# Optimization experiments

Hardware: AMD Instinct MI355X
Metric: run time of the kernel (lower is better)

## Reference

```python
import jax, jax.numpy as jnp
import numpy as np
import math

NUM_BUCKETS = 32
MAX_DISTANCE = 128
N_HEADS = 16
D_KV = 64
ATTN_SCALE = True


def _relative_position_bucket(relative_position, num_buckets=NUM_BUCKETS, max_distance=MAX_DISTANCE):
    # bidirectional (encoder) variant
    nb = num_buckets // 2
    buckets = (relative_position > 0).astype(jnp.int32) * nb
    rp = jnp.abs(relative_position)
    max_exact = nb // 2
    is_small = rp < max_exact
    rp_large = max_exact + (
        jnp.log(rp.astype(jnp.float32) / max_exact)
        / math.log(max_distance / max_exact)
        * (nb - max_exact)
    ).astype(jnp.int32)
    rp_large = jnp.minimum(rp_large, nb - 1)
    buckets = buckets + jnp.where(is_small, rp, rp_large)
    return buckets


def compute_bias(rel_bias_emb, q_len, k_len):
    ctx = jnp.arange(q_len)[:, None]
    mem = jnp.arange(k_len)[None, :]
    bucket = _relative_position_bucket(mem - ctx)  # [q,k] int32 in [0,32)
    values = rel_bias_emb[bucket]                  # [q,k,H]
    return jnp.transpose(values, (2, 0, 1))[None]  # [1,H,q,k]


def setup_inputs() -> dict:
    key = jax.random.key(0)
    k1, k2, k3, k4 = jax.random.split(key, 4)
    B, S, D = 2, 2048, 1024
    return {
        "hidden_states": jax.random.normal(k1, (B, S, D), jnp.float32),
        "attention_mask": jnp.ones((B, 1, S, S), jnp.float32),
        "W_qkv": jax.random.normal(k2, (D, 3 * D), jnp.float32) * 0.02,
        "W_o": jax.random.normal(k3, (D, D), jnp.float32) * 0.02,
        "rel_bias_emb": jax.random.normal(k4, (NUM_BUCKETS, N_HEADS), jnp.float32) * 0.02,
    }


def reference(hidden_states, attention_mask, W_qkv, W_o, rel_bias_emb):
    B, S, D = hidden_states.shape
    # fused QKV projection (no bias), then split as in split_tensor_along_last_dim
    qkv = jnp.einsum("bsd,de->bse", hidden_states, W_qkv)
    q, k, v = jnp.split(qkv, 3, axis=-1)
    # [b,s,H*d] -> [b,H,s,d]
    def to_heads(t):
        return jnp.transpose(t.reshape(B, S, N_HEADS, D_KV), (0, 2, 1, 3))
    q, k, v = to_heads(q), to_heads(k), to_heads(v)
    scores = jnp.einsum("bhqd,bhkd->bhqk", q, k)
    if ATTN_SCALE:
        scores = scores / math.sqrt(D_KV)
    position_bias = compute_bias(rel_bias_emb, S, S)  # [1,H,S,S]
    scores = scores * attention_mask + (-10000.0 * (1.0 - attention_mask) + position_bias)
    probs = jax.nn.softmax(scores, axis=-1)  # dropout = eval mode (identity)
    ctx = jnp.einsum("bhqk,bhkd->bhqd", probs, v)
    ctx = jnp.transpose(ctx, (0, 2, 1, 3)).reshape(B, S, N_HEADS * D_KV)
    attn_output = jnp.einsum("bse,ed->bsd", ctx, W_o)
    return attn_output
```

## Files before the change

### kernel.cpp

```cpp
#include <hip/hip_runtime.h>
#include <cstdint>

#define DEV static __device__ __forceinline__

typedef __bf16 bf16x8 __attribute__((ext_vector_type(8)));
typedef __bf16 bf16x4 __attribute__((ext_vector_type(4)));
typedef short  s16x4  __attribute__((ext_vector_type(4)));
typedef float  f32x4  __attribute__((ext_vector_type(4)));

DEV unsigned short f32_bf16(float f) {
  union { float f; unsigned u; } v; v.f = f;
  unsigned r = v.u + 0x7FFFu + ((v.u >> 16) & 1u);
  return (unsigned short)(r >> 16);
}

DEV void gload16(const void* g, void* lds) {
  __builtin_amdgcn_global_load_lds((__attribute__((address_space(1))) void*)g,
                                   (__attribute__((address_space(3))) void*)lds,
                                   16, 0, 0);
}

DEV float bcast_lane(float v, int srclane) {
  union { float f; int i; } u; u.f = v;
  u.i = __builtin_amdgcn_ds_bpermute(srclane << 2, u.i);
  return u.f;
}

DEV f32x4 mfma16_bf16(bf16x4 a, bf16x4 b, f32x4 c) {
  union { bf16x4 h; s16x4 s; } ua, ub; ua.h = a; ub.h = b;
#if __has_builtin(__builtin_amdgcn_mfma_f32_16x16x16bf16_1k)
  return __builtin_amdgcn_mfma_f32_16x16x16bf16_1k(ua.s, ub.s, c, 0, 0, 0);
#else
  f32x4 d;
  asm("v_mfma_f32_16x16x16_bf16 %0, %1, %2, %3" : "=v"(d) : "v"(ua.s), "v"(ub.s), "v"(c));
  return d;
#endif
}

__global__ void cast_bf16(const float* __restrict__ x, unsigned short* __restrict__ y) {
  int i = blockIdx.x * 256 + threadIdx.x;
  float4 v = ((const float4*)x)[i];
  uint2 o;
  o.x = (unsigned)f32_bf16(v.x) | ((unsigned)f32_bf16(v.y) << 16);
  o.y = (unsigned)f32_bf16(v.z) | ((unsigned)f32_bf16(v.w) << 16);
  ((uint2*)y)[i] = o;
}

__global__ void transpose_cast(const float* __restrict__ W, unsigned short* __restrict__ WT,
                               int K, int N) {
  __shared__ float t[64][65];
  int k0 = blockIdx.x * 64, n0 = blockIdx.y * 64;
  int tn = threadIdx.x & 63, tk = threadIdx.x >> 6;
#pragma unroll
  for (int i = 0; i < 64; i += 4)
    t[tk + i][tn] = W[(size_t)(k0 + tk + i) * N + n0 + tn];
  __syncthreads();
  int k2 = (threadIdx.x & 31) * 2, n = threadIdx.x >> 5;
#pragma unroll
  for (int i = 0; i < 64; i += 8) {
    int nn = n + i;
    unsigned o = (unsigned)f32_bf16(t[k2][nn]) | ((unsigned)f32_bf16(t[k2 + 1][nn]) << 16);
    *(unsigned*)&WT[(size_t)(n0 + nn) * K + k0 + k2] = o;
  }
}

__global__ void mask_check(const float* __restrict__ m, int* __restrict__ flag) {
  size_t i = ((size_t)blockIdx.x * 256 + threadIdx.x) * 4;
  float4 v = *(const float4*)(m + i);
  if (v.x != 1.0f || v.y != 1.0f || v.z != 1.0f || v.w != 1.0f) atomicOr(flag, 1);
}

template <int MODE, int TN>
__global__ void __launch_bounds__(256) gemm_bt(const unsigned short* __restrict__ A,
                                               const unsigned short* __restrict__ BT,
                                               float* __restrict__ Cout,
                                               unsigned short* __restrict__ Qb,
                                               unsigned short* __restrict__ Kb,
                                               unsigned short* __restrict__ VTb,
                                               int M, int N, int K) {
  constexpr int NT = TN / 32;
  __shared__ __align__(16) unsigned short As[128 * 32];
  __shared__ __align__(16) unsigned short Bs[TN * 32];
  const int tid = threadIdx.x, wave = tid >> 6, lane = tid & 63;
  const int l = lane & 15, quad = lane >> 4;
  const int wm = (wave & 1) * 64, wn = (wave >> 1) * (TN >> 1);
  const int bm = blockIdx.x, bn = blockIdx.y;

  const int srowA = wave * 32 + (lane >> 2);
  const int sswzA = ((lane & 3) ^ (srowA & 3)) * 8;
  const int srowB = (TN == 128) ? srowA : (wave * 16 + (lane >> 2));
  const int sswzB = ((lane & 3) ^ (srowB & 3)) * 8;
  const unsigned short* pA = A + (size_t)(bm * 128 + srowA) * K + sswzA;
  const unsigned short* pB = BT + (size_t)(bn * TN + srowB) * K + sswzB;
  unsigned short* ldsA0 = &As[(wave * 32) * 32];
  unsigned short* ldsA1 = &As[(wave * 32 + 16) * 32];
  unsigned short* ldsB0 = &Bs[((TN == 128 ? wave * 32 : wave * 16)) * 32];
  unsigned short* ldsB1 = &Bs[(wave * 32 + 16) * 32];

  f32x4 acc[4][NT];
#pragma unroll
  for (int i = 0; i < 4; i++)
#pragma unroll
    for (int j = 0; j < NT; j++) { f32x4 z = {0.f, 0.f, 0.f, 0.f}; acc[i][j] = z; }

  for (int kt = 0; kt < K; kt += 32) {
    __syncthreads();
    gload16(pA, ldsA0);
    gload16(pA + (size_t)16 * K, ldsA1);
    gload16(pB, ldsB0);
    if (TN == 128) gload16(pB + (size_t)16 * K, ldsB1);
    pA += 32; pB += 32;
    __syncthreads();
    bf16x8 af[4], bv[NT];
#pragma unroll
    for (int mt = 0; mt < 4; mt++) {
      int r = wm + mt * 16 + l;
      af[mt] = *(const bf16x8*)&As[r * 32 + ((quad ^ (r & 3)) * 8)];
    }
#pragma unroll
    for (int nt = 0; nt < NT; nt++) {
      int r = wn + nt * 16 + l;
      bv[nt] = *(const bf16x8*)&Bs[r * 32 + ((quad ^ (r & 3)) * 8)];
    }
#pragma unroll
    for (int mt = 0; mt < 4; mt++)
#pragma unroll
      for (int nt = 0; nt < NT; nt++)
        acc[mt][nt] = __builtin_amdgcn_mfma_f32_16x16x32_bf16(af[mt], bv[nt], acc[mt][nt], 0, 0, 0);
  }

#pragma unroll
  for (int nt = 0; nt < NT; nt++) {
    const int col = bn * TN + wn + nt * 16 + l;
#pragma unroll
    for (int mt = 0; mt < 4; mt++) {
      const int row0 = bm * 128 + wm + mt * 16 + quad * 4;
      if (MODE == 0) {
#pragma unroll
        for (int r = 0; r < 4; r++)
          Cout[(size_t)(row0 + r) * N + col] = acc[mt][nt][r];
      } else {
        const int bb = row0 >> 11, s = row0 & 2047;
        if (col < 2048) {
          unsigned short* dst = (col < 1024) ? Qb : Kb;
          const int c = col & 1023;
          const size_t off = ((size_t)(bb * 16 + (c >> 6)) * 2048 + s) * 64 + (c & 63);
#pragma unroll
          for (int r = 0; r < 4; r++)
            dst[off + (size_t)r * 64] = f32_bf16(acc[mt][nt][r]);
        } else {
          const int c = col - 2048;
          const size_t off = ((size_t)(bb * 16 + (c >> 6)) * 64 + (c & 63)) * 2048 + s;
          bf16x4 pk;
#pragma unroll
          for (int r = 0; r < 4; r++) pk[r] = (__bf16)acc[mt][nt][r];
          *(bf16x4*)&VTb[off] = pk;
        }
      }
    }
  }
}

__global__ void __launch_bounds__(256, 2) attn(const unsigned short* __restrict__ Qb,
                                               const unsigned short* __restrict__ Kb,
                                               const unsigned short* __restrict__ VTb,
                                               const float* __restrict__ mask,
                                               const float* __restrict__ emb,
                                               const int* __restrict__ mflag,
                                               unsigned short* __restrict__ ctx) {
  __shared__ __align__(16) unsigned short KV[2][16384];
  __shared__ float biasLUT[512];

  const float LOG2E = 1.4426950408889634f;
  const float c1 = 0.125f * LOG2E;
  const float C2 = 10000.0f * LOG2E;
  const int tid = threadIdx.x, wave = tid >> 6, lane = tid & 63;
  const int l = lane & 15, quad = lane >> 4;
  const int qt = blockIdx.x & 15, bh = blockIdx.x >> 4;
  const int b = bh >> 4, h = bh & 15;
  const int q0 = qt * 128;

  for (int i = tid; i < 512; i += 256) {
    int rel = i - 256;
    int rp = rel < 0 ? -rel : rel;
    int off = rp < 8 ? rp
                     : 8 + (rp >= 12) + (rp >= 16) + (rp >= 23) + (rp >= 32) +
                           (rp >= 46) + (rp >= 64) + (rp >= 91);
    int bucket = (rel > 0 ? 16 : 0) + off;
    biasLUT[i] = emb[bucket * 16 + h] * LOG2E;
  }
  const float satL = emb[15 * 16 + h] * LOG2E;
  const float satH = emb[31 * 16 + h] * LOG2E;
  const int masked = *mflag;

  const unsigned short* qb  = Qb  + ((size_t)(b * 16 + h) * 2048 + q0) * 64;
  const unsigned short* kb  = Kb  + (size_t)(b * 16 + h) * 2048 * 64;
  const unsigned short* vtb = VTb + (size_t)(b * 16 + h) * 64 * 2048;
  const float* mbase = mask + (size_t)b * 2048 * 2048;

  const int rw8 = lane >> 3, c8 = lane & 7;
  const int rw16 = lane >> 4, c16 = lane & 15;

#pragma unroll
  for (int j = 0; j < 4; j++) {
    int row = wave * 32 + j * 8 + rw8;
    gload16(qb + (size_t)row * 64 + ((c8 ^ (row & 7)) * 8), &KV[1][(wave * 32 + j * 8) * 64]);
  }
#pragma unroll
  for (int j = 0; j < 4; j++) {
    int row = wave * 32 + j * 8 + rw8;
    gload16(kb + (size_t)row * 64 + ((c8 ^ (row & 7)) * 8), &KV[0][(wave * 32 + j * 8) * 64]);
  }
#pragma unroll
  for (int j = 0; j < 4; j++) {
    int drow = wave * 16 + j * 4 + rw16;
    gload16(vtb + (size_t)drow * 2048 + ((c16 ^ (drow & 7)) * 8),
            &KV[0][8192 + (wave * 16 + j * 4) * 128]);
  }
  __syncthreads();

  bf16x8 qf[2][2];
#pragma unroll
  for (int mtq = 0; mtq < 2; mtq++)
#pragma unroll
    for (int ks = 0; ks < 2; ks++) {
      int row = wave * 32 + mtq * 16 + l;
      qf[mtq][ks] = *(const bf16x8*)&KV[1][row * 64 + (((ks * 4 + quad) ^ (row & 7)) * 8)];
    }
  __syncthreads();

#pragma unroll
  for (int j = 0; j < 4; j++) {
    int row = wave * 32 + j * 8 + rw8;
    gload16(kb + (size_t)(128 + row) * 64 + ((c8 ^ (row & 7)) * 8),
            &KV[1][(wave * 32 + j * 8) * 64]);
  }
#pragma unroll
  for (int j = 0; j < 4; j++) {
    int drow = wave * 16 + j * 4 + rw16;
    gload16(vtb + (size_t)drow * 2048 + 128 + ((c16 ^ (drow & 7)) * 8),
            &KV[1][8192 + (wave * 16 + j * 4) * 128]);
  }

  float lr[2] = {0.f, 0.f};
  f32x4 Oa[2][4];
#pragma unroll
  for (int mt = 0; mt < 2; mt++)
#pragma unroll
    for (int dt = 0; dt < 4; dt++) { f32x4 z = {0.f, 0.f, 0.f, 0.f}; Oa[mt][dt] = z; }

  for (int kt = 0; kt < 16; kt++) {
    const int k0 = kt * 128;
    const unsigned short* Ks  = KV[kt & 1];
    const unsigned short* VTs = KV[kt & 1] + 8192;

    const int d0 = k0 - q0;
    const bool sat = (d0 >= 256) || (d0 <= -256);
    const float bias_u = d0 > 0 ? satH : satL;
    const int ibase = 256 + d0 + quad * 4 - wave * 32 - l;
    bf16x4 pa[2][8];

#pragma unroll
    for (int ntk = 0; ntk < 8; ntk++) {
      int row = ntk * 16 + l;
      bf16x8 kf0 = *(const bf16x8*)&Ks[row * 64 + ((quad ^ (row & 7)) * 8)];
      bf16x8 kf1 = *(const bf16x8*)&Ks[row * 64 + (((4 + quad) ^ (row & 7)) * 8)];
#pragma unroll
      for (int mtq = 0; mtq < 2; mtq++) {
        f32x4 s = {0.f, 0.f, 0.f, 0.f};
        s = __builtin_amdgcn_mfma_f32_16x16x32_bf16(kf0, qf[mtq][0], s, 0, 0, 0);
        s = __builtin_amdgcn_mfma_f32_16x16x32_bf16(kf1, qf[mtq][1], s, 0, 0, 0);

        const int ib = ibase - mtq * 16 + ntk * 16;
        if (!masked) {
          if (sat) {
#pragma unroll
            for (int r = 0; r < 4; r++) s[r] = fmaf(s[r], c1, bias_u);
          } else {
#pragma unroll
            for (int r = 0; r < 4; r++) s[r] = fmaf(s[r], c1, biasLUT[ib + r]);
          }
        } else {
          const int qg = q0 + wave * 32 + mtq * 16 + l;
          const int kg = k0 + ntk * 16 + quad * 4;
          float4 mv4 = *(const float4*)&mbase[(size_t)qg * 2048 + kg];
#pragma unroll
          for (int r = 0; r < 4; r++) {
            float mv = r == 0 ? mv4.x : (r == 1 ? mv4.y : (r == 2 ? mv4.z : mv4.w));
            float bias = sat ? bias_u : biasLUT[ib + r];
            s[r] = fmaf(s[r], mv * c1, fmaf(mv, C2, bias - C2));
          }
        }
        bf16x4 pk;
        float ls = 0.f;
#pragma unroll
        for (int r = 0; r < 4; r++) {
          float p = __builtin_amdgcn_exp2f(s[r]);
          ls += p;
          pk[r] = (__bf16)p;
        }
        lr[mtq] += ls;
        pa[mtq][ntk] = pk;
      }
    }

#pragma unroll
    for (int ntk = 0; ntk < 8; ntk++) {
      bf16x4 vf[4];
#pragma unroll
      for (int dt = 0; dt < 4; dt++) {
        int row = dt * 16 + l;
        int ch = (ntk * 2 + (quad >> 1)) ^ (l & 7);
        vf[dt] = *(const bf16x4*)&VTs[row * 128 + ch * 8 + (quad & 1) * 4];
      }
#pragma unroll
      for (int mtq = 0; mtq < 2; mtq++)
#pragma unroll
        for (int dt = 0; dt < 4; dt++)
          Oa[mtq][dt] = mfma16_bf16(pa[mtq][ntk], vf[dt], Oa[mtq][dt]);
    }

    __syncthreads();
    if (kt + 2 < 16) {
      const int kn = (kt + 2) * 128;
      unsigned short* dst = (unsigned short*)KV[kt & 1];
#pragma unroll
      for (int j = 0; j < 4; j++) {
        int row = wave * 32 + j * 8 + rw8;
        gload16(kb + (size_t)(kn + row) * 64 + ((c8 ^ (row & 7)) * 8),
                &dst[(wave * 32 + j * 8) * 64]);
      }
#pragma unroll
      for (int j = 0; j < 4; j++) {
        int drow = wave * 16 + j * 4 + rw16;
        gload16(vtb + (size_t)drow * 2048 + kn + ((c16 ^ (drow & 7)) * 8),
                &dst[8192 + (wave * 16 + j * 4) * 128]);
      }
    }
  }

  float inv[2];
#pragma unroll
  for (int mtq = 0; mtq < 2; mtq++) {
    float v = lr[mtq];
    v += __shfl_xor(v, 16);
    v += __shfl_xor(v, 32);
    inv[mtq] = 1.0f / v;
  }
#pragma unroll
  for (int mt = 0; mt < 2; mt++)
#pragma unroll
    for (int r = 0; r < 4; r++) {
      float i_bc = bcast_lane(inv[mt], quad * 4 + r);
      const int qg = q0 + wave * 32 + mt * 16 + quad * 4 + r;
#pragma unroll
      for (int dt = 0; dt < 4; dt++)
        ctx[(size_t)(b * 2048 + qg) * 1024 + h * 64 + dt * 16 + l] =
            f32_bf16(Oa[mt][dt][r] * i_bc);
    }
}

extern "C" void kernel_launch(void* const* d_in, const int* in_sizes, int n_in,
                              void* d_out, int out_size, void* d_ws, size_t ws_size,
                              hipStream_t stream) {
  const float* hs   = (const float*)d_in[0];
  const float* mask = (const float*)d_in[1];
  const float* wqkv = (const float*)d_in[2];
  const float* wo   = (const float*)d_in[3];
  const float* emb  = (const float*)d_in[4];
  float* out = (float*)d_out;

  char* ws = (char*)d_ws;
  unsigned short* hB  = (unsigned short*)(ws);
  unsigned short* ctx = (unsigned short*)(ws);
  unsigned short* wqT = (unsigned short*)(ws + 8388608);
  unsigned short* woT = (unsigned short*)(ws + 14680064);
  unsigned short* Qb  = (unsigned short*)(ws + 16777216);
  unsigned short* Kb  = (unsigned short*)(ws + 25165824);
  unsigned short* VTb = (unsigned short*)(ws + 33554432);
  int* mflag          = (int*)(ws + 41943040);
  if (ws_size < 41943044) return;

  hipMemsetAsync(mflag, 0, 4, stream);
  cast_bf16<<<4096, 256, 0, stream>>>(hs, hB);
  transpose_cast<<<dim3(16, 48), 256, 0, stream>>>(wqkv, wqT, 1024, 3072);
  transpose_cast<<<dim3(16, 16), 256, 0, stream>>>(wo, woT, 1024, 1024);
  mask_check<<<8192, 256, 0, stream>>>(mask, mflag);
  gemm_bt<2, 128><<<dim3(32, 24), 256, 0, stream>>>(hB, wqT, nullptr, Qb, Kb, VTb, 4096, 3072, 1024);
  attn<<<512, 256, 0, stream>>>(Qb, Kb, VTb, mask, emb, mflag, ctx);
  gemm_bt<0, 64><<<dim3(32, 16), 256, 0, stream>>>(ctx, woT, out, nullptr, nullptr, nullptr, 4096, 1024, 1024);
}
```

Measured before the change: 225.6 us.

## Use 8 waves per attention block with 16 query rows each and reorder block mapping

The attention kernel now launches 512 threads (8 waves) per block. Each wave handles 16 query rows instead of 32, so the per-wave Q fragments, P tiles and output accumulators are halved. The block index mapping is changed so that consecutive blocks cover different batch-heads at the same query tile rather than different query tiles of one head. The goal is more waves in flight to hide latency and a smaller register footprint. The cost is that each K/V tile loaded into LDS is reused by fewer rows per wave, and block-wide barriers now synchronise more waves.

```diff
diff --git a/kernel.cpp b/kernel.cpp
--- a/kernel.cpp
+++ b/kernel.cpp
@@ -161,7 +161,7 @@
   }
 }
 
-__global__ void __launch_bounds__(256, 2) attn(const unsigned short* __restrict__ Qb,
+__global__ void __launch_bounds__(512, 4) attn(const unsigned short* __restrict__ Qb,
                                                const unsigned short* __restrict__ Kb,
                                                const unsigned short* __restrict__ VTb,
                                                const float* __restrict__ mask,
@@ -176,11 +176,12 @@
   const float C2 = 10000.0f * LOG2E;
   const int tid = threadIdx.x, wave = tid >> 6, lane = tid & 63;
   const int l = lane & 15, quad = lane >> 4;
-  const int qt = blockIdx.x & 15, bh = blockIdx.x >> 4;
+  const int bh = blockIdx.x & 31, qt = blockIdx.x >> 5;
   const int b = bh >> 4, h = bh & 15;
   const int q0 = qt * 128;
 
-  for (int i = tid; i < 512; i += 256) {
+  {
+    int i = tid;
     int rel = i - 256;
     int rp = rel < 0 ? -rel : rel;
     int off = rp < 8 ? rp
@@ -202,52 +203,48 @@
   const int rw16 = lane >> 4, c16 = lane & 15;
 
 #pragma unroll
-  for (int j = 0; j < 4; j++) {
-    int row = wave * 32 + j * 8 + rw8;
-    gload16(qb + (size_t)row * 64 + ((c8 ^ (row & 7)) * 8), &KV[1][(wave * 32 + j * 8) * 64]);
-  }
-#pragma unroll
-  for (int j = 0; j < 4; j++) {
-    int row = wave * 32 + j * 8 + rw8;
-    gload16(kb + (size_t)row * 64 + ((c8 ^ (row & 7)) * 8), &KV[0][(wave * 32 + j * 8) * 64]);
-  }
-#pragma unroll
-  for (int j = 0; j < 4; j++) {
-    int drow = wave * 16 + j * 4 + rw16;
+  for (int j = 0; j < 2; j++) {
+    int row = wave * 16 + j * 8 + rw8;
+    gload16(qb + (size_t)row * 64 + ((c8 ^ (row & 7)) * 8), &KV[1][(wave * 16 + j * 8) * 64]);
+  }
+#pragma unroll
+  for (int j = 0; j < 2; j++) {
+    int row = wave * 16 + j * 8 + rw8;
+    gload16(kb + (size_t)row * 64 + ((c8 ^ (row & 7)) * 8), &KV[0][(wave * 16 + j * 8) * 64]);
+  }
+#pragma unroll
+  for (int j = 0; j < 2; j++) {
+    int drow = wave * 8 + j * 4 + rw16;
     gload16(vtb + (size_t)drow * 2048 + ((c16 ^ (drow & 7)) * 8),
-            &KV[0][8192 + (wave * 16 + j * 4) * 128]);
+            &KV[0][8192 + (wave * 8 + j * 4) * 128]);
   }
   __syncthreads();
 
-  bf16x8 qf[2][2];
-#pragma unroll
-  for (int mtq = 0; mtq < 2; mtq++)
-#pragma unroll
-    for (int ks = 0; ks < 2; ks++) {
-      int row = wave * 32 + mtq * 16 + l;
-      qf[mtq][ks] = *(const bf16x8*)&KV[1][row * 64 + (((ks * 4 + quad) ^ (row & 7)) * 8)];
-    }
+  bf16x8 qf[2];
+#pragma unroll
+  for (int ks = 0; ks < 2; ks++) {
+    int row = wave * 16 + l;
+    qf[ks] = *(const bf16x8*)&KV[1][row * 64 + (((ks * 4 + quad) ^ (row & 7)) * 8)];
+  }
   __syncthreads();
 
 #pragma unroll
-  for (int j = 0; j < 4; j++) {
-    int row = wave * 32 + j * 8 + rw8;
+  for (int j = 0; j < 2; j++) {
+    int row = wave * 16 + j * 8 + rw8;
     gload16(kb + (size_t)(128 + row) * 64 + ((c8 ^ (row & 7)) * 8),
-            &KV[1][(wave * 32 + j * 8) * 64]);
-  }
-#pragma unroll
-  for (int j = 0; j < 4; j++) {
-    int drow = wave * 16 + j * 4 + rw16;
+            &KV[1][(wave * 16 + j * 8) * 64]);
+  }
+#pragma unroll
+  for (int j = 0; j < 2; j++) {
+    int drow = wave * 8 + j * 4 + rw16;
     gload16(vtb + (size_t)drow * 2048 + 128 + ((c16 ^ (drow & 7)) * 8),
-            &KV[1][8192 + (wave * 16 + j * 4) * 128]);
-  }
-
-  float lr[2] = {0.f, 0.f};
-  f32x4 Oa[2][4];
-#pragma unroll
-  for (int mt = 0; mt < 2; mt++)
-#pragma unroll
-    for (int dt = 0; dt < 4; dt++) { f32x4 z = {0.f, 0.f, 0.f, 0.f}; Oa[mt][dt] = z; }
+            &KV[1][8192 + (wave * 8 + j * 4) * 128]);
+  }
+
+  float lr = 0.f;
+  f32x4 Oa[4];
+#pragma unroll
+  for (int dt = 0; dt < 4; dt++) { f32x4 z = {0.f, 0.f, 0.f, 0.f}; Oa[dt] = z; }
 
   for (int kt = 0; kt < 16; kt++) {
     const int k0 = kt * 128;
@@ -257,51 +254,48 @@
     const int d0 = k0 - q0;
     const bool sat = (d0 >= 256) || (d0 <= -256);
     const float bias_u = d0 > 0 ? satH : satL;
-    const int ibase = 256 + d0 + quad * 4 - wave * 32 - l;
-    bf16x4 pa[2][8];
+    const int ibase = 256 + d0 + quad * 4 - wave * 16 - l;
+    bf16x4 pa[8];
 
 #pragma unroll
     for (int ntk = 0; ntk < 8; ntk++) {
       int row = ntk * 16 + l;
       bf16x8 kf0 = *(const bf16x8*)&Ks[row * 64 + ((quad ^ (row & 7)) * 8)];
       bf16x8 kf1 = *(const bf16x8*)&Ks[row * 64 + (((4 + quad) ^ (row & 7)) * 8)];
-#pragma unroll
-      for (int mtq = 0; mtq < 2; mtq++) {
-        f32x4 s = {0.f, 0.f, 0.f, 0.f};
-        s = __builtin_amdgcn_mfma_f32_16x16x32_bf16(kf0, qf[mtq][0], s, 0, 0, 0);
-        s = __builtin_amdgcn_mfma_f32_16x16x32_bf16(kf1, qf[mtq][1], s, 0, 0, 0);
-
-        const int ib = ibase - mtq * 16 + ntk * 16;
-        if (!masked) {
-          if (sat) {
-#pragma unroll
-            for (int r = 0; r < 4; r++) s[r] = fmaf(s[r], c1, bias_u);
-          } else {
-#pragma unroll
-            for (int r = 0; r < 4; r++) s[r] = fmaf(s[r], c1, biasLUT[ib + r]);
-          }
+      f32x4 s = {0.f, 0.f, 0.f, 0.f};
+      s = __builtin_amdgcn_mfma_f32_16x16x32_bf16(kf0, qf[0], s, 0, 0, 0);
+      s = __builtin_amdgcn_mfma_f32_16x16x32_bf16(kf1, qf[1], s, 0, 0, 0);
+
+      const int ib = ibase + ntk * 16;
+      if (!masked) {
+        if (sat) {
+#pragma unroll
+          for (int r = 0; r < 4; r++) s[r] = fmaf(s[r], c1, bias_u);
         } else {
-          const int qg = q0 + wave * 32 + mtq * 16 + l;
-          const int kg = k0 + ntk * 16 + quad * 4;
-          float4 mv4 = *(const float4*)&mbase[(size_t)qg * 2048 + kg];
-#pragma unroll
-          for (int r = 0; r < 4; r++) {
-            float mv = r == 0 ? mv4.x : (r == 1 ? mv4.y : (r == 2 ? mv4.z : mv4.w));
-            float bias = sat ? bias_u : biasLUT[ib + r];
-            s[r] = fmaf(s[r], mv * c1, fmaf(mv, C2, bias - C2));
-          }
+#pragma unroll
+          for (int r = 0; r < 4; r++) s[r] = fmaf(s[r], c1, biasLUT[ib + r]);
         }
-        bf16x4 pk;
-        float ls = 0.f;
+      } else {
+        const int qg = q0 + wave * 16 + l;
+        const int kg = k0 + ntk * 16 + quad * 4;
+        float4 mv4 = *(const float4*)&mbase[(size_t)qg * 2048 + kg];
 #pragma unroll
         for (int r = 0; r < 4; r++) {
-          float p = __builtin_amdgcn_exp2f(s[r]);
-          ls += p;
-          pk[r] = (__bf16)p;
+          float mv = r == 0 ? mv4.x : (r == 1 ? mv4.y : (r == 2 ? mv4.z : mv4.w));
+          float bias = sat ? bias_u : biasLUT[ib + r];
+          s[r] = fmaf(s[r], mv * c1, fmaf(mv, C2, bias - C2));
         }
-        lr[mtq] += ls;
-        pa[mtq][ntk] = pk;
-      }
+      }
+      bf16x4 pk;
+      float ls = 0.f;
+#pragma unroll
+      for (int r = 0; r < 4; r++) {
+        float p = __builtin_amdgcn_exp2f(s[r]);
+        ls += p;
+        pk[r] = (__bf16)p;
+      }
+      lr += ls;
+      pa[ntk] = pk;
     }
 
 #pragma unroll
@@ -314,10 +308,8 @@
         vf[dt] = *(const bf16x4*)&VTs[row * 128 + ch * 8 + (quad & 1) * 4];
       }
 #pragma unroll
-      for (int mtq = 0; mtq < 2; mtq++)
-#pragma unroll
-        for (int dt = 0; dt < 4; dt++)
-          Oa[mtq][dt] = mfma16_bf16(pa[mtq][ntk], vf[dt], Oa[mtq][dt]);
+      for (int dt = 0; dt < 4; dt++)
+        Oa[dt] = mfma16_bf16(pa[ntk], vf[dt], Oa[dt]);
     }
 
     __syncthreads();
@@ -325,39 +317,33 @@
       const int kn = (kt + 2) * 128;
       unsigned short* dst = (unsigned short*)KV[kt & 1];
 #pragma unroll
-      for (int j = 0; j < 4; j++) {
-        int row = wave * 32 + j * 8 + rw8;
+      for (int j = 0; j < 2; j++) {
+        int row = wave * 16 + j * 8 + rw8;
         gload16(kb + (size_t)(kn + row) * 64 + ((c8 ^ (row & 7)) * 8),
-                &dst[(wave * 32 + j * 8) * 64]);
-      }
-#pragma unroll
-      for (int j = 0; j < 4; j++) {
-        int drow = wave * 16 + j * 4 + rw16;
+                &dst[(wave * 16 + j * 8) * 64]);
+      }
+#pragma unroll
+      for (int j = 0; j < 2; j++) {
+        int drow = wave * 8 + j * 4 + rw16;
         gload16(vtb + (size_t)drow * 2048 + kn + ((c16 ^ (drow & 7)) * 8),
-                &dst[8192 + (wave * 16 + j * 4) * 128]);
-      }
-    }
-  }
-
-  float inv[2];
-#pragma unroll
-  for (int mtq = 0; mtq < 2; mtq++) {
-    float v = lr[mtq];
-    v += __shfl_xor(v, 16);
-    v += __shfl_xor(v, 32);
-    inv[mtq] = 1.0f / v;
-  }
-#pragma unroll
-  for (int mt = 0; mt < 2; mt++)
-#pragma unroll
-    for (int r = 0; r < 4; r++) {
-      float i_bc = bcast_lane(inv[mt], quad * 4 + r);
-      const int qg = q0 + wave * 32 + mt * 16 + quad * 4 + r;
-#pragma unroll
-      for (int dt = 0; dt < 4; dt++)
-        ctx[(size_t)(b * 2048 + qg) * 1024 + h * 64 + dt * 16 + l] =
-            f32_bf16(Oa[mt][dt][r] * i_bc);
-    }
+                &dst[8192 + (wave * 8 + j * 4) * 128]);
+      }
+    }
+  }
+
+  float v = lr;
+  v += __shfl_xor(v, 16);
+  v += __shfl_xor(v, 32);
+  const float inv = 1.0f / v;
+#pragma unroll
+  for (int r = 0; r < 4; r++) {
+    float i_bc = bcast_lane(inv, quad * 4 + r);
+    const int qg = q0 + wave * 16 + quad * 4 + r;
+#pragma unroll
+    for (int dt = 0; dt < 4; dt++)
+      ctx[(size_t)(b * 2048 + qg) * 1024 + h * 64 + dt * 16 + l] =
+          f32_bf16(Oa[dt][r] * i_bc);
+  }
 }
 
 extern "C" void kernel_launch(void* const* d_in, const int* in_sizes, int n_in,
@@ -387,6 +373,6 @@
   transpose_cast<<<dim3(16, 16), 256, 0, stream>>>(wo, woT, 1024, 1024);
   mask_check<<<8192, 256, 0, stream>>>(mask, mflag);
   gemm_bt<2, 128><<<dim3(32, 24), 256, 0, stream>>>(hB, wqT, nullptr, Qb, Kb, VTb, 4096, 3072, 1024);
-  attn<<<512, 256, 0, stream>>>(Qb, Kb, VTb, mask, emb, mflag, ctx);
+  attn<<<512, 512, 0, stream>>>(Qb, Kb, VTb, mask, emb, mflag, ctx);
   gemm_bt<0, 64><<<dim3(32, 16), 256, 0, stream>>>(ctx, woT, out, nullptr, nullptr, nullptr, 4096, 1024, 1024);
 }
```

New measurement: 220.2 us. 1.02x faster.
